# Optimization experiments

Hardware: AMD Instinct MI355X
Metric: run time of the kernel (lower is better)

## Reference

```python
import jax, jax.numpy as jnp
import numpy as np


def setup_inputs() -> dict:
    key = jax.random.key(0)
    k1, k2, k3, k4, k5 = jax.random.split(key, 5)
    B, N, E, C_in, C_out, K = 64, 4096, 16, 64, 64, 3
    return {
        "x": jax.random.normal(k1, (B, N, C_in), dtype=jnp.float32),
        "adj_matrix": jax.random.normal(k2, (N, E), dtype=jnp.float32),
        "adj_embeddings": jax.random.normal(k3, (E, N), dtype=jnp.float32),
        "weights": jax.random.normal(k4, (K, C_in, C_out), dtype=jnp.float32) * 0.1,
        "bias": jax.random.normal(k5, (C_out,), dtype=jnp.float32) * 0.1,
    }


def reference(x, adj_matrix, adj_embeddings, weights, bias):
    # x: [B, N, C_in]; adj_matrix: [N, E]; adj_embeddings: [E, N]
    N = adj_matrix.shape[0]
    cheb_k = weights.shape[0]
    # adaptive adjacency: softmax(relu(adj @ emb), axis=1) -> [N, N]
    supports = jax.nn.softmax(jax.nn.relu(adj_matrix @ adj_embeddings), axis=1)
    # Chebyshev polynomial recursion: T0 = I, T1 = supports,
    # Tk = 2*supports @ T_{k-1} - T_{k-2}
    support_set = [jnp.eye(N, dtype=supports.dtype), supports]
    for _ in range(2, cheb_k):
        support_set.append(2.0 * supports @ support_set[-1] - support_set[-2])
    supports_k = jnp.stack(support_set, axis=0)  # [K, N, N]
    # aggregate: [K,N,M] x [B,M,C] -> [B,N,K,C]
    x_g = jnp.einsum("knm,bmc->bnkc", supports_k, x)
    # mix: [B,N,K,Cin] x [K,Cin,Cout] -> [B,N,Cout]
    return jnp.einsum("bnki,kio->bno", x_g, weights) + bias
```

## Files before the change

kernel.cpp:

```cpp
#include <hip/hip_runtime.h>


typedef __bf16 bf16;
typedef __bf16 bf16x8 __attribute__((ext_vector_type(8)));
typedef float f32x4 __attribute__((ext_vector_type(4)));

__device__ __forceinline__ void async_lds16(const void* g, void* l) {
  __builtin_amdgcn_global_load_lds((const __attribute__((address_space(1))) void*)g,
                                   (__attribute__((address_space(3))) void*)l, 16, 0, 0);
}

__global__ __launch_bounds__(256) void build_wcat_k(const float* __restrict__ w, bf16* __restrict__ Wc) {
  int idx = blockIdx.x * 256 + threadIdx.x;
  if (idx >= 64 * 192) return;
  int o = idx / 192, kk = idx - o * 192;
  int k = kk >> 6, i = kk & 63;
  float v;
  if (k == 0)      v = w[i * 64 + o] - w[2 * 4096 + i * 64 + o];
  else if (k == 1) v = w[4096 + i * 64 + o];
  else             v = 2.f * w[2 * 4096 + i * 64 + o];
  Wc[idx] = (bf16)v;
}

__global__ __launch_bounds__(256) void supports_k(const float* __restrict__ adj,
                                                  const float* __restrict__ emb,
                                                  bf16* __restrict__ S) {
  __shared__ float sadj[8][16];
  __shared__ float sred[4];
  const int tid = threadIdx.x;
  const int n0 = blockIdx.x * 8;
  if (tid < 128) sadj[tid >> 4][tid & 15] = adj[n0 * 16 + tid];
  __syncthreads();
  for (int r = 0; r < 8; ++r) {
    float vals[16];
    float mx = 0.f;
    #pragma unroll
    for (int it = 0; it < 16; ++it) {
      const int j = it * 256 + tid;
      float v = 0.f;
      #pragma unroll
      for (int e = 0; e < 16; ++e) v = fmaf(sadj[r][e], emb[e * 4096 + j], v);
      v = fmaxf(v, 0.f);
      vals[it] = v;
      mx = fmaxf(mx, v);
    }
    #pragma unroll
    for (int off = 32; off > 0; off >>= 1) mx = fmaxf(mx, __shfl_xor(mx, off, 64));
    if ((tid & 63) == 0) sred[tid >> 6] = mx;
    __syncthreads();
    mx = fmaxf(fmaxf(sred[0], sred[1]), fmaxf(sred[2], sred[3]));
    float sum = 0.f;
    #pragma unroll
    for (int it = 0; it < 16; ++it) {
      float ev = __expf(vals[it] - mx);
      vals[it] = ev;
      sum += ev;
    }
    #pragma unroll
    for (int off = 32; off > 0; off >>= 1) sum += __shfl_xor(sum, off, 64);
    __syncthreads();
    if ((tid & 63) == 0) sred[tid >> 6] = sum;
    __syncthreads();
    const float inv = 1.f / (sred[0] + sred[1] + sred[2] + sred[3]);
    bf16* Srow = S + (n0 + r) * 4096;
    #pragma unroll
    for (int it = 0; it < 16; ++it) Srow[it * 256 + tid] = (bf16)(vals[it] * inv);
    __syncthreads();
  }
}

__global__ __launch_bounds__(256) void xpose_x_k(const float* __restrict__ x, bf16* __restrict__ Xt) {
  __shared__ float tile[64][65];
  const int tid = threadIdx.x;
  const int mt = blockIdx.x, b = blockIdx.y;
  const float* src = x + (b * 4096 + mt * 64) * 64;
  #pragma unroll
  for (int it = 0; it < 16; ++it) {
    const int idx = it * 256 + tid;
    tile[idx >> 6][idx & 63] = src[idx];
  }
  __syncthreads();
  #pragma unroll
  for (int it = 0; it < 16; ++it) {
    const int idx = it * 256 + tid;
    const int rr = idx >> 6, cc = idx & 63;
    Xt[(b * 64 + rr) * 4096 + mt * 64 + cc] = (bf16)tile[cc][rr];
  }
}

__global__ __launch_bounds__(256) void transpose_bf16_k(const bf16* __restrict__ in, bf16* __restrict__ outT) {
  __shared__ bf16 tile[64][65];
  const int tid = threadIdx.x;
  const int ti = blockIdx.x & 63, tj = blockIdx.x >> 6;
  #pragma unroll
  for (int it = 0; it < 16; ++it) {
    const int idx = it * 256 + tid;
    tile[idx >> 6][idx & 63] = in[(ti * 64 + (idx >> 6)) * 4096 + tj * 64 + (idx & 63)];
  }
  __syncthreads();
  #pragma unroll
  for (int it = 0; it < 16; ++it) {
    const int idx = it * 256 + tid;
    const int rr = idx >> 6, cc = idx & 63;
    outT[(tj * 64 + rr) * 4096 + ti * 64 + cc] = tile[cc][rr];
  }
}

__global__ __launch_bounds__(256) void gemm_bt_k(const bf16* __restrict__ A, const bf16* __restrict__ Bt,
                                                 bf16* __restrict__ C) {
  __shared__ bf16 As[128 * 64];
  __shared__ bf16 Bs[128 * 64];
  const int tid = threadIdx.x;
  const int tm = blockIdx.x & 31, tn = blockIdx.x >> 5;
  const int rowBase = tm * 128, colBase = tn * 128;

  const int r = tid >> 3;
  const int kp = ((tid & 7) ^ (r & 7)) * 8;
  const bf16* gA = A + (rowBase + r) * 4096 + kp;
  const bf16* gB = Bt + (colBase + r) * 4096 + kp;

  const int lane = tid & 63, wv = tid >> 6;
  bf16* ldsA = As + wv * 512;
  bf16* ldsB = Bs + wv * 512;

  const int t16 = lane & 15, quad = lane >> 4;
  const int sz7 = t16 & 7;
  const int wm = (wv >> 1) * 64, wn = (wv & 1) * 64;
  const bf16* pA = As + (wm + t16) * 64;
  const bf16* pB = Bs + (wn + t16) * 64;

  f32x4 acc[4][4];
  #pragma unroll
  for (int i = 0; i < 4; ++i)
    #pragma unroll
    for (int j = 0; j < 4; ++j) acc[i][j] = (f32x4){0.f, 0.f, 0.f, 0.f};

  for (int k0 = 0; k0 < 4096; k0 += 64) {
    __syncthreads();
    #pragma unroll
    for (int p = 0; p < 4; ++p) {
      async_lds16(gA + p * 32 * 4096 + k0, ldsA + p * 2048);
      async_lds16(gB + p * 32 * 4096 + k0, ldsB + p * 2048);
    }
    __syncthreads();
    #pragma unroll
    for (int ks = 0; ks < 2; ++ks) {
      const int ch = ((ks * 4 + quad) ^ sz7) << 3;
      bf16x8 af[4], bfv[4];
      #pragma unroll
      for (int i = 0; i < 4; ++i) af[i] = *(const bf16x8*)(pA + i * 16 * 64 + ch);
      #pragma unroll
      for (int j = 0; j < 4; ++j) bfv[j] = *(const bf16x8*)(pB + j * 16 * 64 + ch);
      #pragma unroll
      for (int i = 0; i < 4; ++i)
        #pragma unroll
        for (int j = 0; j < 4; ++j)
          acc[i][j] = __builtin_amdgcn_mfma_f32_16x16x32_bf16(af[i], bfv[j], acc[i][j], 0, 0, 0);
    }
  }

  #pragma unroll
  for (int i = 0; i < 4; ++i) {
    const int row0 = rowBase + wm + i * 16 + quad * 4;
    #pragma unroll
    for (int j = 0; j < 4; ++j) {
      const int col = colBase + wn + j * 16 + t16;
      #pragma unroll
      for (int rr = 0; rr < 4; ++rr)
        C[(row0 + rr) * 4096 + col] = (bf16)acc[i][j][rr];
    }
  }
}

__global__ __launch_bounds__(256) void mix_k(const float* __restrict__ x, const bf16* __restrict__ XG1,
                                             const bf16* __restrict__ XG2, const bf16* __restrict__ Wc,
                                             const float* __restrict__ bias, float* __restrict__ out) {
  __shared__ bf16 sW[64 * 200];
  const int tid = threadIdx.x;
  const int nt = blockIdx.x, b = blockIdx.y;
  {
    const int rw = tid >> 2, part = tid & 3;
    #pragma unroll
    for (int v = 0; v < 6; ++v)
      *(bf16x8*)(sW + rw * 200 + part * 48 + v * 8) = *(const bf16x8*)(Wc + rw * 192 + part * 48 + v * 8);
  }
  __syncthreads();

  const int lane = tid & 63, wv = tid >> 6;
  const int t16 = lane & 15, quad = lane >> 4;
  const int nBase = nt * 128 + wv * 32;

  f32x4 acc[2][4];
  #pragma unroll
  for (int i = 0; i < 2; ++i)
    #pragma unroll
    for (int j = 0; j < 4; ++j) acc[i][j] = (f32x4){0.f, 0.f, 0.f, 0.f};

  #pragma unroll
  for (int ch = 0; ch < 6; ++ch) {
    bf16x8 a[2];
    #pragma unroll
    for (int i = 0; i < 2; ++i) {
      const int row = nBase + i * 16 + t16;
      if (ch < 2) {
        const float* p = x + (b * 4096 + row) * 64 + ch * 32 + quad * 8;
        float4 f0 = *(const float4*)p;
        float4 f1 = *(const float4*)(p + 4);
        bf16x8 t;
        t[0] = (bf16)f0.x; t[1] = (bf16)f0.y; t[2] = (bf16)f0.z; t[3] = (bf16)f0.w;
        t[4] = (bf16)f1.x; t[5] = (bf16)f1.y; t[6] = (bf16)f1.z; t[7] = (bf16)f1.w;
        a[i] = t;
      } else {
        const bf16* src = (ch < 4) ? XG1 : XG2;
        a[i] = *(const bf16x8*)(src + row * 4096 + b * 64 + (ch & 1) * 32 + quad * 8);
      }
    }
    #pragma unroll
    for (int j = 0; j < 4; ++j) {
      bf16x8 wf = *(const bf16x8*)(sW + (j * 16 + t16) * 200 + ch * 32 + quad * 8);
      #pragma unroll
      for (int i = 0; i < 2; ++i)
        acc[i][j] = __builtin_amdgcn_mfma_f32_16x16x32_bf16(a[i], wf, acc[i][j], 0, 0, 0);
    }
  }

  #pragma unroll
  for (int j = 0; j < 4; ++j) {
    const float bb = bias[j * 16 + t16];
    #pragma unroll
    for (int i = 0; i < 2; ++i) {
      const int n0 = nBase + i * 16 + quad * 4;
      #pragma unroll
      for (int rr = 0; rr < 4; ++rr)
        out[(b * 4096 + n0 + rr) * 64 + j * 16 + t16] = acc[i][j][rr] + bb;
    }
  }
}

extern "C" void kernel_launch(void* const* d_in, const int* in_sizes, int n_in,
                              void* d_out, int out_size, void* d_ws, size_t ws_size,
                              hipStream_t stream) {
  const float* x    = (const float*)d_in[0];
  const float* adj  = (const float*)d_in[1];
  const float* emb  = (const float*)d_in[2];
  const float* w    = (const float*)d_in[3];
  const float* bias = (const float*)d_in[4];
  float* out = (float*)d_out;

  char* ws = (char*)d_ws;
  const size_t SZ = (size_t)4096 * 4096 * sizeof(bf16);
  bf16* S    = (bf16*)(ws);
  bf16* XG1  = (bf16*)(ws + SZ);
  bf16* XG2  = (bf16*)(ws + 2 * SZ);
  bf16* XBUF = (bf16*)(ws + 3 * SZ);
  bf16* Wc   = (bf16*)(ws + 4 * SZ);

  build_wcat_k<<<48, 256, 0, stream>>>(w, Wc);
  supports_k<<<512, 256, 0, stream>>>(adj, emb, S);
  xpose_x_k<<<dim3(64, 64), 256, 0, stream>>>(x, XBUF);
  gemm_bt_k<<<1024, 256, 0, stream>>>(S, XBUF, XG1);
  transpose_bf16_k<<<4096, 256, 0, stream>>>(XG1, XBUF);
  gemm_bt_k<<<1024, 256, 0, stream>>>(S, XBUF, XG2);
  mix_k<<<dim3(32, 64), 256, 0, stream>>>(x, XG1, XG2, Wc, bias, out);
}
```

Baseline: 473.7 us.

## Replace GEMM with 256x256-tile double-buffered pipelined MFMA kernel

Swaps the 128x128, single-buffered GEMM for a 256x256-tile kernel with 8 waves. It double-buffers LDS, interleaves async global->LDS loads with register-prefetched MFMA groups under explicit vmcnt waits and barriers, and raises wave priority around MFMA. It also remaps block IDs to group tiles for L2 locality. The goal is to hide global load latency and cut the LDS/global traffic per FLOP. In exchange it uses more registers and LDS per block, and the hand-written barrier and wait ordering is fragile.

```diff
diff --git a/kernel.cpp b/kernel.cpp
--- a/kernel.cpp
+++ b/kernel.cpp
@@ -9,6 +9,15 @@
   __builtin_amdgcn_global_load_lds((const __attribute__((address_space(1))) void*)g,
                                    (__attribute__((address_space(3))) void*)l, 16, 0, 0);
 }
+
+#define FENCE() asm volatile("" ::: "memory")
+#define BAR()                          \
+  do {                                 \
+    FENCE();                           \
+    __builtin_amdgcn_s_barrier();      \
+    FENCE();                           \
+  } while (0)
+#define WAIT_VM(n) asm volatile("s_waitcnt vmcnt(" #n ")" ::: "memory")
 
 __global__ __launch_bounds__(256) void build_wcat_k(const float* __restrict__ w, bf16* __restrict__ Wc) {
   int idx = blockIdx.x * 256 + threadIdx.x;
@@ -106,68 +115,125 @@
   }
 }
 
-__global__ __launch_bounds__(256) void gemm_bt_k(const bf16* __restrict__ A, const bf16* __restrict__ Bt,
-                                                 bf16* __restrict__ C) {
-  __shared__ bf16 As[128 * 64];
-  __shared__ bf16 Bs[128 * 64];
-  const int tid = threadIdx.x;
-  const int tm = blockIdx.x & 31, tn = blockIdx.x >> 5;
-  const int rowBase = tm * 128, colBase = tn * 128;
-
-  const int r = tid >> 3;
-  const int kp = ((tid & 7) ^ (r & 7)) * 8;
-  const bf16* gA = A + (rowBase + r) * 4096 + kp;
-  const bf16* gB = Bt + (colBase + r) * 4096 + kp;
-
-  const int lane = tid & 63, wv = tid >> 6;
-  bf16* ldsA = As + wv * 512;
-  bf16* ldsB = Bs + wv * 512;
-
+__global__ __launch_bounds__(512, 2) void gemm256_k(const bf16* __restrict__ A,
+                                                    const bf16* __restrict__ Bt,
+                                                    bf16* __restrict__ C) {
+  __shared__ bf16 As[2][2][256][32];
+  __shared__ bf16 Bs[2][2][256][32];
+
+  const int tid = threadIdx.x;
+  const int bid = blockIdx.x;
+  const int wg = (bid & 7) * 32 + (bid >> 3);
+  const int tm = wg >> 4, tn = wg & 15;
+  const int rowBase = tm * 256, colBase = tn * 256;
+
+  const int wv = tid >> 6, lane = tid & 63;
+  const int wm = wv >> 2, wn = wv & 3;
   const int t16 = lane & 15, quad = lane >> 4;
-  const int sz7 = t16 & 7;
-  const int wm = (wv >> 1) * 64, wn = (wv & 1) * 64;
-  const bf16* pA = As + (wm + t16) * 64;
-  const bf16* pB = Bs + (wn + t16) * 64;
-
-  f32x4 acc[4][4];
-  #pragma unroll
-  for (int i = 0; i < 4; ++i)
+  const int wv16 = wv * 16;
+  const int q8 = quad * 8;
+  const int wm128 = wm * 128;
+  const int wn64 = wn * 64;
+
+  const int sr = tid >> 2, sc = (tid & 3) * 8;
+  const bf16* gA = A + (size_t)(rowBase + sr) * 4096 + sc;
+  const bf16* gB = Bt + (size_t)(colBase + sr) * 4096 + sc;
+
+  f32x4 acc[8][4];
+  #pragma unroll
+  for (int i = 0; i < 8; ++i)
     #pragma unroll
     for (int j = 0; j < 4; ++j) acc[i][j] = (f32x4){0.f, 0.f, 0.f, 0.f};
 
-  for (int k0 = 0; k0 < 4096; k0 += 64) {
-    __syncthreads();
-    #pragma unroll
-    for (int p = 0; p < 4; ++p) {
-      async_lds16(gA + p * 32 * 4096 + k0, ldsA + p * 2048);
-      async_lds16(gB + p * 32 * 4096 + k0, ldsB + p * 2048);
-    }
-    __syncthreads();
-    #pragma unroll
-    for (int ks = 0; ks < 2; ++ks) {
-      const int ch = ((ks * 4 + quad) ^ sz7) << 3;
-      bf16x8 af[4], bfv[4];
-      #pragma unroll
-      for (int i = 0; i < 4; ++i) af[i] = *(const bf16x8*)(pA + i * 16 * 64 + ch);
-      #pragma unroll
-      for (int j = 0; j < 4; ++j) bfv[j] = *(const bf16x8*)(pB + j * 16 * 64 + ch);
-      #pragma unroll
-      for (int i = 0; i < 4; ++i)
-        #pragma unroll
-        for (int j = 0; j < 4; ++j)
-          acc[i][j] = __builtin_amdgcn_mfma_f32_16x16x32_bf16(af[i], bfv[j], acc[i][j], 0, 0, 0);
-    }
-  }
-
-  #pragma unroll
-  for (int i = 0; i < 4; ++i) {
-    const int row0 = rowBase + wm + i * 16 + quad * 4;
+  auto stA = [&](int buf, int s, int k0) {
+    async_lds16(gA + k0 + s * 32, &As[buf][s][wv16][0]);
+    async_lds16(gA + 524288 + k0 + s * 32, &As[buf][s][128 + wv16][0]);
+  };
+  auto stB = [&](int buf, int s, int k0) {
+    async_lds16(gB + k0 + s * 32, &Bs[buf][s][wv16][0]);
+    async_lds16(gB + 524288 + k0 + s * 32, &Bs[buf][s][128 + wv16][0]);
+  };
+
+  bf16x8 Ra[4], Rb[4], B0[4], B1[4];
+  auto rdA = [&](bf16x8* R, int buf, int s, int g) {
+    #pragma unroll
+    for (int i = 0; i < 4; ++i)
+      R[i] = *(const bf16x8*)&As[buf][s][wm128 + (g * 4 + i) * 16 + t16][q8];
+  };
+  auto rdB = [&](bf16x8* R, int buf, int s) {
+    #pragma unroll
+    for (int j = 0; j < 4; ++j)
+      R[j] = *(const bf16x8*)&Bs[buf][s][wn64 + j * 16 + t16][q8];
+  };
+  auto mfma16 = [&](int g, const bf16x8* R, const bf16x8* Bv) {
+    __builtin_amdgcn_s_setprio(1);
+    #pragma unroll
+    for (int i = 0; i < 4; ++i)
+      #pragma unroll
+      for (int j = 0; j < 4; ++j)
+        acc[g * 4 + i][j] =
+            __builtin_amdgcn_mfma_f32_16x16x32_bf16(R[i], Bv[j], acc[g * 4 + i][j], 0, 0, 0);
+    __builtin_amdgcn_s_setprio(0);
+  };
+
+  stB(0, 0, 0); stA(0, 0, 0); stB(0, 1, 0); stA(0, 1, 0);
+  stB(1, 0, 64); stA(1, 0, 64); stB(1, 1, 64);
+  WAIT_VM(6);
+  BAR();
+  rdA(Ra, 0, 0, 0);
+  rdB(B0, 0, 0);
+
+  for (int it = 0; it < 31; ++it) {
+    const int kb = it * 128;
+    rdA(Rb, 0, 0, 1); stA(1, 1, kb + 64);
+    BAR(); mfma16(0, Ra, B0); BAR();
+    rdA(Ra, 0, 1, 0); rdB(B1, 0, 1); stB(0, 0, kb + 128);
+    BAR(); mfma16(1, Rb, B0); BAR();
+    rdA(Rb, 0, 1, 1); stA(0, 0, kb + 128);
+    BAR(); mfma16(0, Ra, B1); BAR();
+    stB(0, 1, kb + 128); WAIT_VM(6);
+    BAR();
+    rdA(Ra, 1, 0, 0); rdB(B0, 1, 0);
+    mfma16(1, Rb, B1); BAR();
+    rdA(Rb, 1, 0, 1); stA(0, 1, kb + 128);
+    BAR(); mfma16(0, Ra, B0); BAR();
+    rdA(Ra, 1, 1, 0); rdB(B1, 1, 1); stB(1, 0, kb + 192);
+    BAR(); mfma16(1, Rb, B0); BAR();
+    rdA(Rb, 1, 1, 1); stA(1, 0, kb + 192);
+    BAR(); mfma16(0, Ra, B1); BAR();
+    stB(1, 1, kb + 192); WAIT_VM(6);
+    BAR();
+    rdA(Ra, 0, 0, 0); rdB(B0, 0, 0);
+    mfma16(1, Rb, B1); BAR();
+  }
+
+  rdA(Rb, 0, 0, 1); stA(1, 1, 4032);
+  BAR(); mfma16(0, Ra, B0); BAR();
+  rdA(Ra, 0, 1, 0); rdB(B1, 0, 1);
+  BAR(); mfma16(1, Rb, B0); BAR();
+  rdA(Rb, 0, 1, 1);
+  BAR(); mfma16(0, Ra, B1); BAR();
+  WAIT_VM(0);
+  BAR();
+  rdA(Ra, 1, 0, 0); rdB(B0, 1, 0);
+  mfma16(1, Rb, B1); BAR();
+  rdA(Rb, 1, 0, 1);
+  mfma16(0, Ra, B0);
+  rdA(Ra, 1, 1, 0); rdB(B1, 1, 1);
+  mfma16(1, Rb, B0);
+  rdA(Rb, 1, 1, 1);
+  mfma16(0, Ra, B1);
+  mfma16(1, Rb, B1);
+
+  #pragma unroll
+  for (int i = 0; i < 8; ++i) {
+    const int row0 = rowBase + wm128 + i * 16 + quad * 4;
     #pragma unroll
     for (int j = 0; j < 4; ++j) {
-      const int col = colBase + wn + j * 16 + t16;
+      const int col = colBase + wn64 + j * 16 + t16;
       #pragma unroll
       for (int rr = 0; rr < 4; ++rr)
-        C[(row0 + rr) * 4096 + col] = (bf16)acc[i][j][rr];
+        C[(size_t)(row0 + rr) * 4096 + col] = (bf16)acc[i][j][rr];
     }
   }
 }
@@ -258,8 +324,8 @@
   build_wcat_k<<<48, 256, 0, stream>>>(w, Wc);
   supports_k<<<512, 256, 0, stream>>>(adj, emb, S);
   xpose_x_k<<<dim3(64, 64), 256, 0, stream>>>(x, XBUF);
-  gemm_bt_k<<<1024, 256, 0, stream>>>(S, XBUF, XG1);
+  gemm256_k<<<256, 512, 0, stream>>>(S, XBUF, XG1);
   transpose_bf16_k<<<4096, 256, 0, stream>>>(XG1, XBUF);
-  gemm_bt_k<<<1024, 256, 0, stream>>>(S, XBUF, XG2);
+  gemm256_k<<<256, 512, 0, stream>>>(S, XBUF, XG2);
   mix_k<<<dim3(32, 64), 256, 0, stream>>>(x, XG1, XG2, Wc, bias, out);
 }
```

Measured after the change: 454.0 us. 1.04x faster.
